# Performance work log

Hardware: AMD Instinct MI355X
Metric: run time of the kernel (lower is better)

## Reference

```python
import jax, jax.numpy as jnp
import numpy as np

N0 = 100000; E0 = 1600000; N1 = 100000; E1 = 1600000; G = 512
F0 = 93; F1 = 43
BN_EPS = 1e-5


def setup_inputs() -> dict:
    key = jax.random.key(0)
    ks = jax.random.split(key, 20)
    p = lambda i, shape: jax.random.normal(ks[i], shape, jnp.float32) * 0.02
    return {
        "x_0": jax.random.normal(ks[0], (N0, F0), jnp.float32),
        "x_1": jax.random.normal(ks[1], (N1, F1), jnp.float32),
        "edge_index_0": jax.random.randint(ks[2], (2, E0), 0, N0, jnp.int32),
        "edge_index_1": jax.random.randint(ks[3], (2, E1), 0, N1, jnp.int32),
        "batch_0": jnp.sort(jax.random.randint(ks[4], (N0,), 0, G, jnp.int32)),
        "batch_1": jnp.sort(jax.random.randint(ks[5], (N1,), 0, G, jnp.int32)),
        "w_c1": p(6, (F0, F0)), "b_c1": jnp.zeros((F0,), jnp.float32),
        "w_c2": p(7, (F0, F0 * 10)), "b_c2": jnp.zeros((F0 * 10,), jnp.float32),
        "w_c3": p(8, (F1, F1)), "b_c3": jnp.zeros((F1,), jnp.float32),
        "w_c4": p(9, (F1, F1 * 10)), "b_c4": jnp.zeros((F1 * 10,), jnp.float32),
        "g0_w1": p(10, (F0 * 10 * 2, 1024)), "g0_b1": jnp.zeros((1024,), jnp.float32),
        "g0_w2": p(11, (1024, 512)), "g0_b2": jnp.zeros((512,), jnp.float32),
        "g0_bn_g": jnp.ones((512,), jnp.float32), "g0_bn_b": jnp.zeros((512,), jnp.float32),
        "g1_w1": p(12, (F1 * 10 * 2, 1024)), "g1_b1": jnp.zeros((1024,), jnp.float32),
        "g1_w2": p(13, (1024, 512)), "g1_b2": jnp.zeros((512,), jnp.float32),
        "g1_bn_g": jnp.ones((512,), jnp.float32), "g1_bn_b": jnp.zeros((512,), jnp.float32),
        "f0_w1": p(14, (512, 256)), "f0_b1": jnp.zeros((256,), jnp.float32),
        "f0_w2": p(15, (256, 2)), "f0_b2": jnp.zeros((2,), jnp.float32),
        "f1_w1": p(16, (512, 256)), "f1_b1": jnp.zeros((256,), jnp.float32),
        "f1_w2": p(17, (256, 2)), "f1_b2": jnp.zeros((2,), jnp.float32),
    }


def gin_conv(x, edge_index, W, b):
    # GINConv(eps=0): nn(x + sum_{j->i} x_j); messages from src=edge_index[0] to dst=edge_index[1]
    agg = jax.ops.segment_sum(x[edge_index[0]], edge_index[1], num_segments=x.shape[0])
    return (x + agg) @ W + b


def pool_mean_max(x, batch):
    cnt = jax.ops.segment_sum(jnp.ones((x.shape[0], 1), x.dtype), batch, num_segments=G)
    mean = jax.ops.segment_sum(x, batch, num_segments=G) / jnp.maximum(cnt, 1.0)
    mx = jax.ops.segment_max(x, batch, num_segments=G)
    mx = jnp.where(cnt > 0, mx, 0.0)
    return jnp.concatenate([mean, mx], axis=1)


def batchnorm(x, g, b):
    m = x.mean(axis=0)
    v = x.var(axis=0)
    return g * (x - m) / jnp.sqrt(v + BN_EPS) + b


def branch(x, ei, batch, w_a, b_a, w_b, b_b, w1, b1, w2, b2, bn_g, bn_b):
    h = jax.nn.relu(gin_conv(x, ei, w_a, b_a))
    h = jax.nn.relu(gin_conv(h, ei, w_b, b_b))
    h = pool_mean_max(h, batch)              # [G, 2*10*F] ; PairNorm(mode='None') is identity
    h = jax.nn.relu(h @ w1 + b1)             # dropout: eval mode (identity)
    h = h @ w2 + b2
    return batchnorm(h, bn_g, bn_b)          # [G, 512]


def reference(x_0, x_1, edge_index_0, edge_index_1, batch_0, batch_1,
              w_c1, b_c1, w_c2, b_c2, w_c3, b_c3, w_c4, b_c4,
              g0_w1, g0_b1, g0_w2, g0_b2, g0_bn_g, g0_bn_b,
              g1_w1, g1_b1, g1_w2, g1_b2, g1_bn_g, g1_bn_b,
              f0_w1, f0_b1, f0_w2, f0_b2, f1_w1, f1_b1, f1_w2, f1_b2):
    x_g_0 = branch(x_0, edge_index_0, batch_0, w_c1, b_c1, w_c2, b_c2,
                   g0_w1, g0_b1, g0_w2, g0_b2, g0_bn_g, g0_bn_b)
    z = jax.nn.relu(x_g_0 @ f0_w1 + f0_b1) @ f0_w2 + f0_b2
    x_g_1 = branch(x_1, edge_index_1, batch_1, w_c3, b_c3, w_c4, b_c4,
                   g1_w1, g1_b1, g1_w2, g1_b2, g1_bn_g, g1_bn_b)
    z1 = jax.nn.relu(x_g_1 @ f1_w1 + f1_b1) @ f1_w2 + f1_b2
    return (z, x_g_0, x_g_1, z1)
```

## Files before the change

### kernel.cpp

```cpp
#include <hip/hip_runtime.h>
#include <hip/hip_bf16.h>

#define N0 100000
#define E0C 1600000
#define N1 100000
#define E1C 1600000
#define GCONST 512
#define F0C 93
#define F1C 43
#define OC0 (F0C * 10)
#define OC1 (F1C * 10)
#define BN_EPS 1e-5f
#define NBKT 391

typedef __attribute__((ext_vector_type(8))) short short8;
typedef __attribute__((ext_vector_type(4))) float floatx4;

static __device__ __forceinline__ unsigned short f2bf(float f) {
    unsigned u = __float_as_uint(f);
    unsigned r = (u + 0x7FFF + ((u >> 16) & 1)) >> 16;
    return (unsigned short)r;
}
static __device__ __forceinline__ float bf2f(unsigned short u) {
    return __uint_as_float(((unsigned)u) << 16);
}
static __device__ __forceinline__ void split_bf(float v, unsigned short& h, unsigned short& l) {
    h = f2bf(v);
    l = f2bf(v - bf2f(h));
}

__global__ __launch_bounds__(256) void bucket_count2_kernel(const int* __restrict__ ei0,
                                                            const int* __restrict__ ei1,
                                                            int E, int* __restrict__ btot2) {
    const int* ei = blockIdx.y ? ei1 : ei0;
    int* btot = btot2 + blockIdx.y * 512;
    __shared__ int h[NBKT];
    int t = threadIdx.x;
    for (int i = t; i < NBKT; i += 256) h[i] = 0;
    __syncthreads();
    int base = blockIdx.x * 2048;
#pragma unroll
    for (int i = 0; i < 8; ++i) {
        int e = base + i * 256 + t;
        if (e < E) atomicAdd(&h[ei[E + e] >> 8], 1);
    }
    __syncthreads();
    for (int i = t; i < NBKT; i += 256) {
        int c = h[i];
        if (c) atomicAdd(&btot[i], c);
    }
}

__global__ __launch_bounds__(512) void bucket_scan2_kernel(const int* __restrict__ btot2,
                                                           int* __restrict__ bbase2,
                                                           int* __restrict__ bcur2) {
    const int* btot = btot2 + blockIdx.x * 512;
    int* bbase = bbase2 + blockIdx.x * 512;
    int* bcur  = bcur2 + blockIdx.x * 512;
    __shared__ int sh[512];
    int t = threadIdx.x;
    int v = (t < NBKT) ? btot[t] : 0;
    sh[t] = v;
    __syncthreads();
    for (int o = 1; o < 512; o <<= 1) {
        int add = (t >= o) ? sh[t - o] : 0;
        __syncthreads();
        sh[t] += add;
        __syncthreads();
    }
    if (t < NBKT) {
        int ex = sh[t] - v;
        bbase[t] = ex;
        bcur[t] = ex;
    }
    if (t == NBKT) bbase[t] = sh[NBKT - 1];
}

__global__ __launch_bounds__(256) void edge_bucket2_kernel(const int* __restrict__ ei0,
                                                           const int* __restrict__ ei1,
                                                           int E, int* __restrict__ bcur2,
                                                           int2* __restrict__ st0,
                                                           int2* __restrict__ st1) {
    const int* ei = blockIdx.y ? ei1 : ei0;
    int* bcur = bcur2 + blockIdx.y * 512;
    int2* staging = blockIdx.y ? st1 : st0;
    __shared__ int hist[NBKT];
    __shared__ int gbase[NBKT];
    int t = threadIdx.x;
    for (int i = t; i < NBKT; i += 256) hist[i] = 0;
    __syncthreads();
    int base = blockIdx.x * 2048;
    int srcv[8], dstv[8];
#pragma unroll
    for (int i = 0; i < 8; ++i) {
        int e = base + i * 256 + t;
        if (e < E) { srcv[i] = ei[e]; dstv[i] = ei[E + e]; }
        else dstv[i] = -1;
    }
#pragma unroll
    for (int i = 0; i < 8; ++i)
        if (dstv[i] >= 0) atomicAdd(&hist[dstv[i] >> 8], 1);
    __syncthreads();
    for (int i = t; i < NBKT; i += 256) {
        int c = hist[i];
        gbase[i] = c ? atomicAdd(&bcur[i], c) : 0;
        hist[i] = 0;
    }
    __syncthreads();
#pragma unroll
    for (int i = 0; i < 8; ++i) {
        if (dstv[i] >= 0) {
            int b = dstv[i] >> 8;
            int lofs = atomicAdd(&hist[b], 1);
            staging[gbase[b] + lofs] = make_int2(srcv[i], dstv[i]);
        }
    }
}

static __device__ __forceinline__ void csr_build_dev(int b, const int2* __restrict__ staging,
                                                     const int* __restrict__ bbase, int N,
                                                     int* __restrict__ rowptr,
                                                     int* __restrict__ col) {
    __shared__ int h[256];
    __shared__ int sc[256];
    int t = threadIdx.x;
    int s = bbase[b], e = bbase[b + 1];
    h[t] = 0;
    __syncthreads();
    for (int i = s + t; i < e; i += 256)
        atomicAdd(&h[staging[i].y & 255], 1);
    __syncthreads();
    int v = h[t];
    sc[t] = v;
    __syncthreads();
    for (int o = 1; o < 256; o <<= 1) {
        int add = (t >= o) ? sc[t - o] : 0;
        __syncthreads();
        sc[t] += add;
        __syncthreads();
    }
    int ex = s + (sc[t] - v);
    int node = (b << 8) + t;
    if (node <= N) rowptr[node] = ex;
    __syncthreads();
    sc[t] = ex;
    __syncthreads();
    for (int i = s + t; i < e; i += 256) {
        int2 ed = staging[i];
        int pos = atomicAdd(&sc[ed.y & 255], 1);
        col[pos] = ed.x;
    }
}

__global__ __launch_bounds__(256) void misc_kernel(const int* __restrict__ bat0,
                                                   const int* __restrict__ bat1,
                                                   int* __restrict__ st0,
                                                   int* __restrict__ st1,
                                                   const float* __restrict__ Wc1,
                                                   const float* __restrict__ Wc2,
                                                   const float* __restrict__ Wc3,
                                                   const float* __restrict__ Wc4,
                                                   unsigned short* __restrict__ Ta0,
                                                   unsigned short* __restrict__ Tb0,
                                                   unsigned short* __restrict__ Ta1,
                                                   unsigned short* __restrict__ Tb1,
                                                   int* __restrict__ btot2,
                                                   unsigned short* __restrict__ p0h,
                                                   unsigned short* __restrict__ p0l,
                                                   unsigned short* __restrict__ p1h,
                                                   unsigned short* __restrict__ p1l) {
    int bid = blockIdx.x;
    int t = threadIdx.x;
    if (bid < 6) {
        int branch = bid / 3;
        const int* batch = branch ? bat1 : bat0;
        int* starts = branch ? st1 : st0;
        int g = (bid % 3) * 256 + t;
        if (g > GCONST) return;
        if (g == GCONST) { starts[GCONST] = N0; return; }
        int lo = 0, hi = N0;
        while (lo < hi) {
            int mid = (lo + hi) >> 1;
            if (batch[mid] < g) lo = mid + 1; else hi = mid;
        }
        starts[g] = lo;
    } else if (bid < 2054) {
        int idx = bid - 6;
        int cfg = idx >> 9;
        int c = (idx & 511) * 2 + (t >> 7);
        int k = t & 127;
        const float* W; unsigned short* T; int OCr, Fr, KP, RB;
        switch (cfg) {
            case 0:  W = Wc1; T = Ta0; OCr = 93;  Fr = 93; KP = 96; RB = 96;   break;
            case 1:  W = Wc2; T = Tb0; OCr = 930; Fr = 93; KP = 96; RB = 1024; break;
            case 2:  W = Wc3; T = Ta1; OCr = 43;  Fr = 43; KP = 64; RB = 48;   break;
            default: W = Wc4; T = Tb1; OCr = 430; Fr = 43; KP = 64; RB = 512;  break;
        }
        if (c >= RB || k >= KP) return;
        unsigned short v = 0;
        if (c < OCr && k < Fr) v = f2bf(W[(size_t)k * OCr + c]);
        T[(size_t)c * KP + k] = v;
    } else if (bid < 2058) {
        int i = (bid - 2054) * 256 + t;
        if (i < 1024) btot2[i] = 0;
    } else if (bid < 2178) {
        int i = (bid - 2058) * 256 + t;
        if (i >= GCONST * 60) return;
        int g = i / 60, c = 1860 + (i - g * 60);
        p0h[(size_t)g * 1920 + c] = 0;
        p0l[(size_t)g * 1920 + c] = 0;
    } else {
        int i = (bid - 2178) * 256 + t;
        if (i >= GCONST * 36) return;
        int g = i / 36, c = 860 + (i - g * 36);
        p1h[(size_t)g * 896 + c] = 0;
        p1l[(size_t)g * 896 + c] = 0;
    }
}

static __device__ __forceinline__ void wsplit_dev(int k0, int c0,
                                                  const float* __restrict__ W,
                                                  unsigned short* __restrict__ Th,
                                                  unsigned short* __restrict__ Tl,
                                                  int K, int N, int KP) {
    __shared__ float tile[32][33];
    int tx = threadIdx.x & 31, ty = threadIdx.x >> 5;
    for (int r = ty; r < 32; r += 8) {
        int k = k0 + r;
        tile[r][tx] = (k < K) ? W[(size_t)k * N + c0 + tx] : 0.f;
    }
    __syncthreads();
    for (int r = ty; r < 32; r += 8) {
        int c = c0 + r;
        float v = tile[tx][r];
        unsigned short h, l;
        split_bf(v, h, l);
        Th[(size_t)c * KP + k0 + tx] = h;
        Tl[(size_t)c * KP + k0 + tx] = l;
    }
}


template<int KP, int CH, int GR>
static __device__ __forceinline__ void gather_dev(int nb, unsigned short* __restrict__ t,
                                                  const unsigned short* __restrict__ x,
                                                  const int* __restrict__ rowptr,
                                                  const int* __restrict__ col, int N) {
    int wave = threadIdx.x >> 6, lane = threadIdx.x & 63;
    int node = nb * 4 + wave;
    if (node >= N) return;
    int g = lane / CH;
    int c = lane - g * CH;
    bool act = (g < GR);
    int s = rowptr[node], e = rowptr[node + 1];
    float acc[8] = {0.f, 0.f, 0.f, 0.f, 0.f, 0.f, 0.f, 0.f};
    int j = act ? (s - 1 + g) : e;
    int src0 = node;
    if (j >= s && j < e) src0 = col[j];
    while (j < e) {
        int jb = j + GR;
        int jc = jb + GR;
        int srcb = (jb < e) ? col[jb] : 0;
        int srcc = (jc < e) ? col[jc] : 0;
        short8 v0 = *(const short8*)(x + (size_t)src0 * KP + c * 8);
#pragma unroll
        for (int i = 0; i < 8; ++i) acc[i] += bf2f((unsigned short)v0[i]);
        if (jb < e) {
            short8 v1 = *(const short8*)(x + (size_t)srcb * KP + c * 8);
#pragma unroll
            for (int i = 0; i < 8; ++i) acc[i] += bf2f((unsigned short)v1[i]);
        }
        j = jc; src0 = srcc;
    }
    if (GR == 8) {
#pragma unroll
        for (int i = 0; i < 8; ++i) {
            float v = acc[i];
            v += __shfl_xor(v, 8);
            v += __shfl_xor(v, 16);
            v += __shfl_xor(v, 32);
            acc[i] = v;
        }
    } else {
#pragma unroll
        for (int i = 0; i < 8; ++i) {
            float v = acc[i];
            float v1 = __shfl(v, lane + CH);
            float v2 = __shfl(v, lane + 2 * CH);
            float v3 = __shfl(v, lane + 3 * CH);
            float v4 = __shfl(v, lane + 4 * CH);
            acc[i] = v + v1 + v2 + v3 + v4;
        }
    }
    if (lane < CH) {
        short8 o;
#pragma unroll
        for (int i = 0; i < 8; ++i) o[i] = (short)f2bf(acc[i]);
        *(short8*)(t + (size_t)node * KP + lane * 8) = o;
    }
}

template<int KP, int KS, int NT>
static __device__ __forceinline__ void conv1_dev(int nb, const unsigned short* __restrict__ t,
                                                 const unsigned short* __restrict__ Wt,
                                                 const float* __restrict__ bias,
                                                 unsigned short* __restrict__ y,
                                                 int NC, int N) {
    int wave = threadIdx.x >> 6, lane = threadIdx.x & 63;
    int quad = lane >> 4, l15 = lane & 15;
    int r0 = (nb * 4 + wave) * 16;
    const short8 z8 = {0, 0, 0, 0, 0, 0, 0, 0};
    short8 a[KS];
    int arow = r0 + l15;
#pragma unroll
    for (int ks = 0; ks < KS; ++ks)
        a[ks] = (arow < N) ? *(const short8*)(t + (size_t)arow * KP + ks * 32 + quad * 8) : z8;
#pragma unroll
    for (int nt = 0; nt < NT; ++nt) {
        int colb = nt * 16 + l15;
        floatx4 c = {0.f, 0.f, 0.f, 0.f};
#pragma unroll
        for (int ks = 0; ks < KS; ++ks) {
            short8 b = *(const short8*)(Wt + (size_t)colb * KP + ks * 32 + quad * 8);
            c = __builtin_amdgcn_mfma_f32_16x16x32_bf16(a[ks], b, c, 0, 0, 0);
// ... 131 lines not shown
    int col0 = c0 + l15, col1 = c0 + 16 + l15;
    float bc0 = bias[col0], bc1 = bias[col1];
#pragma unroll
    for (int r = 0; r < 4; ++r) {
        int row = r0 + quad * 4 + r;
        float v0 = acc0[r] + bc0;
        float v1 = acc1[r] + bc1;
        if (MODE != 1) { v0 = fmaxf(v0, 0.f); v1 = fmaxf(v1, 0.f); }
        if (MODE == 0) {
            unsigned short h, l;
            split_bf(v0, h, l);
            Ch[(size_t)row * Ncols + col0] = h; Cl[(size_t)row * Ncols + col0] = l;
            split_bf(v1, h, l);
            Ch[(size_t)row * Ncols + col1] = h; Cl[(size_t)row * Ncols + col1] = l;
        } else {
            Cf[(size_t)row * Ncols + col0] = v0;
            Cf[(size_t)row * Ncols + col1] = v1;
        }
    }
}

static __device__ __forceinline__ void bn_dev(int c, const float* __restrict__ p,
                                              const float* __restrict__ gamma,
                                              const float* __restrict__ beta,
                                              float* __restrict__ outp,
                                              unsigned short* __restrict__ oh,
                                              unsigned short* __restrict__ ol) {
    __shared__ float ls[256], ls2[256];
    int t = threadIdx.x;
    float v0 = p[(size_t)t * 512 + c];
    float v1 = p[(size_t)(t + 256) * 512 + c];
    ls[t] = v0 + v1;
    ls2[t] = v0 * v0 + v1 * v1;
    __syncthreads();
    for (int st = 128; st > 0; st >>= 1) {
        if (t < st) { ls[t] += ls[t + st]; ls2[t] += ls2[t + st]; }
        __syncthreads();
    }
    if (t == 0) {
        float m = ls[0] / 512.f;
        float var = ls2[0] / 512.f - m * m;
        ls[0] = m;
        ls2[0] = 1.f / sqrtf(var + BN_EPS);
    }
    __syncthreads();
    float m = ls[0], iv = ls2[0];
    float g = gamma[c], b = beta[c];
    float w0 = g * (v0 - m) * iv + b;
    float w1 = g * (v1 - m) * iv + b;
    outp[(size_t)t * 512 + c] = w0;
    outp[(size_t)(t + 256) * 512 + c] = w1;
    unsigned short h, l;
    split_bf(w0, h, l);
    oh[(size_t)t * 512 + c] = h; ol[(size_t)t * 512 + c] = l;
    split_bf(w1, h, l);
    oh[(size_t)(t + 256) * 512 + c] = h; ol[(size_t)(t + 256) * 512 + c] = l;
}

static __device__ __forceinline__ void head2_dev(int nb, const float* __restrict__ h,
                                                 const float* __restrict__ w2,
                                                 const float* __restrict__ b2,
                                                 float* __restrict__ z, int M) {
    int wave = threadIdx.x >> 6, lane = threadIdx.x & 63;
    int row = nb * 4 + wave;
    if (row >= M) return;
    float4 hv = *(const float4*)(h + (size_t)row * 256 + lane * 4);
    const float* wp = w2 + lane * 8;
    float s0 = hv.x * wp[0] + hv.y * wp[2] + hv.z * wp[4] + hv.w * wp[6];
    float s1 = hv.x * wp[1] + hv.y * wp[3] + hv.z * wp[5] + hv.w * wp[7];
#pragma unroll
    for (int offd = 32; offd >= 1; offd >>= 1) {
        s0 += __shfl_down(s0, offd);
        s1 += __shfl_down(s1, offd);
    }
    if (lane == 0) {
        z[(size_t)row * 2 + 0] = s0 + b2[0];
        z[(size_t)row * 2 + 1] = s1 + b2[1];
    }
}


__global__ __launch_bounds__(256) void f0_kernel(const int2* __restrict__ st0,
                                                 const int2* __restrict__ st1,
                                                 const int* __restrict__ bbase2,
                                                 int* __restrict__ rp0, int* __restrict__ rp1,
                                                 int* __restrict__ c0, int* __restrict__ c1,
                                                 unsigned short* __restrict__ xb0,
                                                 const float* __restrict__ x0,
                                                 unsigned short* __restrict__ xb1,
                                                 const float* __restrict__ x1) {
    int bid = blockIdx.x;
    if (bid < 2 * NBKT) {
        int branch = bid >= NBKT;
        csr_build_dev(branch ? bid - NBKT : bid,
                      branch ? st1 : st0, bbase2 + branch * 512, N0,
                      branch ? rp1 : rp0, branch ? c1 : c0);
    } else if (bid < 2 * NBKT + 50000) {
        int b = bid - 2 * NBKT;
        int node = b * 2 + (threadIdx.x >> 7);
        int f = threadIdx.x & 127;
        if (node < N0 && f < 96)
            xb0[(size_t)node * 96 + f] = (f < 93) ? f2bf(x0[(size_t)node * 93 + f]) : (unsigned short)0;
    } else {
        int b = bid - 2 * NBKT - 50000;
        int node = b * 4 + (threadIdx.x >> 6);
        int f = threadIdx.x & 63;
        if (node < N1)
            xb1[(size_t)node * 64 + f] = (f < 43) ? f2bf(x1[(size_t)node * 43 + f]) : (unsigned short)0;
    }
}

__global__ __launch_bounds__(256) void f1_kernel(unsigned short* __restrict__ tb,
                                                 const unsigned short* __restrict__ xb0,
                                                 const int* __restrict__ rowptr0,
                                                 const int* __restrict__ col0,
                                                 const float* g0_w1, const float* g0_w2,
                                                 const float* f0_w1,
                                                 const float* g1_w1, const float* g1_w2,
                                                 const float* f1_w1,
                                                 unsigned short* bt1h0, unsigned short* bt1l0,
                                                 unsigned short* bt2h0, unsigned short* bt2l0,
                                                 unsigned short* bt3h0, unsigned short* bt3l0,
                                                 unsigned short* bt1h1, unsigned short* bt1l1,
                                                 unsigned short* bt2h1, unsigned short* bt2l1,
                                                 unsigned short* bt3h1, unsigned short* bt3l1) {
    int bid = blockIdx.x;
    if (bid < 25000) {
        gather_dev<96, 12, 5>(bid, tb, xb0, rowptr0, col0, N0);
        return;
    }
    int w = bid - 25000;
    if (w < 1920)      wsplit_dev((w % 60) * 32, (w / 60) * 32, g0_w1, bt1h0, bt1l0, 1860, 1024, 1920);
    else if (w < 2432) { w -= 1920; wsplit_dev((w % 32) * 32, (w / 32) * 32, g0_w2, bt2h0, bt2l0, 1024, 512, 1024); }
    else if (w < 2560) { w -= 2432; wsplit_dev((w % 16) * 32, (w / 16) * 32, f0_w1, bt3h0, bt3l0, 512, 256, 512); }
    else if (w < 3456) { w -= 2560; wsplit_dev((w % 28) * 32, (w / 28) * 32, g1_w1, bt1h1, bt1l1, 860, 1024, 896); }
    else if (w < 3968) { w -= 3456; wsplit_dev((w % 32) * 32, (w / 32) * 32, g1_w2, bt2h1, bt2l1, 1024, 512, 1024); }
    else               { w -= 3968; wsplit_dev((w % 16) * 32, (w / 16) * 32, f1_w1, bt3h1, bt3l1, 512, 256, 512); }
}

__global__ __launch_bounds__(256) void f2_kernel(unsigned short* __restrict__ t1,
                                                 const unsigned short* __restrict__ xb1,
                                                 const int* __restrict__ rowptr1,
                                                 const int* __restrict__ col1,
                                                 const unsigned short* __restrict__ tb,
                                                 const unsigned short* __restrict__ wt_a0,
                                                 const float* __restrict__ b_c1,
                                                 unsigned short* __restrict__ yb) {
    int bid = blockIdx.x;
    if (bid < 25000)
        gather_dev<64, 8, 8>(bid, t1, xb1, rowptr1, col1, N1);
    else
        conv1_dev<96, 3, 6>(bid - 25000, tb, wt_a0, b_c1, yb, 93, N0);
}

__global__ __launch_bounds__(256) void f3_kernel(unsigned short* __restrict__ tb,
                                                 const unsigned short* __restrict__ yb,
                                                 const int* __restrict__ rowptr0,
                                                 const int* __restrict__ col0,
                                                 const unsigned short* __restrict__ t1,
                                                 const unsigned short* __restrict__ wt_a1,
                                                 const float* __restrict__ b_c3,
                                                 unsigned short* __restrict__ y1) {
    int bid = blockIdx.x;
    if (bid < 25000)
        gather_dev<96, 12, 5>(bid, tb, yb, rowptr0, col0, N0);
    else
        conv1_dev<64, 2, 3>(bid - 25000, t1, wt_a1, b_c3, y1, 43, N1);
}

__global__ __launch_bounds__(256) void f4_kernel(unsigned short* __restrict__ t1,
                                                 const unsigned short* __restrict__ y1,
                                                 const int* __restrict__ rowptr1,
                                                 const int* __restrict__ col1,
                                                 const unsigned short* __restrict__ tb,
                                                 const unsigned short* __restrict__ wt_b0,
                                                 const float* __restrict__ b_c2,
                                                 const int* __restrict__ starts0,
                                                 unsigned short* __restrict__ p0h,
                                                 unsigned short* __restrict__ p0l) {
    int bid = blockIdx.x;
    if (bid < 25000)
        gather_dev<64, 8, 8>(bid, t1, y1, rowptr1, col1, N1);
    else {
        int b = bid - 25000;
        conv2_pool_dev<96, 3>(b & 3, b >> 2, tb, wt_b0, b_c2, starts0, p0h, p0l, OC0, 1920);
    }
}

__global__ __launch_bounds__(256) void f5_kernel(const unsigned short* __restrict__ t1,
                                                 const unsigned short* __restrict__ wt_b1,
                                                 const float* __restrict__ b_c4,
                                                 const int* __restrict__ starts1,
                                                 unsigned short* __restrict__ p1h,
                                                 unsigned short* __restrict__ p1l,
                                                 const unsigned short* __restrict__ p0h,
                                                 const unsigned short* __restrict__ p0l,
                                                 const unsigned short* __restrict__ bt1h0,
                                                 const unsigned short* __restrict__ bt1l0,
                                                 const float* __restrict__ g0_b1,
                                                 unsigned short* __restrict__ m1h0,
                                                 unsigned short* __restrict__ m1l0) {
    int bid = blockIdx.x;
    if (bid < 1024)
        conv2_pool_dev<64, 2>(bid & 1, bid >> 1, t1, wt_b1, b_c4, starts1, p1h, p1l, OC1, 896);
    else {
        int b = bid - 1024;
        gemm3x_dev<0>(b & 15, b >> 4, 16, p0h, p0l, bt1h0, bt1l0, g0_b1,
                      nullptr, m1h0, m1l0, 1920);
    }
}

__global__ __launch_bounds__(256) void f6_kernel(const unsigned short* __restrict__ p1h,
                                                 const unsigned short* __restrict__ p1l,
                                                 const unsigned short* __restrict__ bt1h1,
                                                 const unsigned short* __restrict__ bt1l1,
                                                 const float* __restrict__ g1_b1,
                                                 unsigned short* __restrict__ m1h1,
                                                 unsigned short* __restrict__ m1l1,
                                                 const unsigned short* __restrict__ m1h0,
                                                 const unsigned short* __restrict__ m1l0,
                                                 const unsigned short* __restrict__ bt2h0,
                                                 const unsigned short* __restrict__ bt2l0,
                                                 const float* __restrict__ g0_b2,
                                                 float* __restrict__ pbn0) {
    int bid = blockIdx.x;
    if (bid < 256)
        gemm3x_dev<0>(bid & 15, bid >> 4, 16, p1h, p1l, bt1h1, bt1l1, g1_b1,
                      nullptr, m1h1, m1l1, 896);
    else {
        int b = bid - 256;
        gemm3x_dev<1>(b & 7, b >> 3, 8, m1h0, m1l0, bt2h0, bt2l0, g0_b2,
                      pbn0, nullptr, nullptr, 1024);
    }
}

__global__ __launch_bounds__(256) void f7_kernel(const unsigned short* __restrict__ m1h1,
                                                 const unsigned short* __restrict__ m1l1,
                                                 const unsigned short* __restrict__ bt2h1,
                                                 const unsigned short* __restrict__ bt2l1,
                                                 const float* __restrict__ g1_b2,
                                                 float* __restrict__ pbn1,
                                                 const float* __restrict__ pbn0,
                                                 const float* __restrict__ g0_bn_g,
                                                 const float* __restrict__ g0_bn_b,
                                                 float* __restrict__ out_xg0,
                                                 unsigned short* __restrict__ xgh0,
                                                 unsigned short* __restrict__ xgl0) {
    int bid = blockIdx.x;
    if (bid < 128)
        gemm3x_dev<1>(bid & 7, bid >> 3, 8, m1h1, m1l1, bt2h1, bt2l1, g1_b2,
                      pbn1, nullptr, nullptr, 1024);
    else
        bn_dev(bid - 128, pbn0, g0_bn_g, g0_bn_b, out_xg0, xgh0, xgl0);
}

__global__ __launch_bounds__(256) void f8_kernel(const float* __restrict__ pbn1,
                                                 const float* __restrict__ g1_bn_g,
                                                 const float* __restrict__ g1_bn_b,
                                                 float* __restrict__ out_xg1,
                                                 unsigned short* __restrict__ xgh1,
                                                 unsigned short* __restrict__ xgl1,
                                                 const unsigned short* __restrict__ xgh0,
                                                 const unsigned short* __restrict__ xgl0,
                                                 const unsigned short* __restrict__ bt3h0,
                                                 const unsigned short* __restrict__ bt3l0,
                                                 const float* __restrict__ f0_b1,
                                                 float* __restrict__ hbuf0) {
    int bid = blockIdx.x;
    if (bid < 512)
        bn_dev(bid, pbn1, g1_bn_g, g1_bn_b, out_xg1, xgh1, xgl1);
    else {
        int b = bid - 512;
        gemm3x_dev<2>(b & 3, b >> 2, 4, xgh0, xgl0, bt3h0, bt3l0, f0_b1,
                      hbuf0, nullptr, nullptr, 512);
    }
}

__global__ __launch_bounds__(256) void f9_kernel(const unsigned short* __restrict__ xgh1,
                                                 const unsigned short* __restrict__ xgl1,
                                                 const unsigned short* __restrict__ bt3h1,
                                                 const unsigned short* __restrict__ bt3l1,
                                                 const float* __restrict__ f1_b1,
                                                 float* __restrict__ hbuf1,
                                                 const float* __restrict__ hbuf0,
                                                 const float* __restrict__ f0_w2,
                                                 const float* __restrict__ f0_b2,
                                                 float* __restrict__ out_z) {
    int bid = blockIdx.x;
    if (bid < 64)
        gemm3x_dev<2>(bid & 3, bid >> 2, 4, xgh1, xgl1, bt3h1, bt3l1, f1_b1,
                      hbuf1, nullptr, nullptr, 512);
    else
        head2_dev(bid - 64, hbuf0, f0_w2, f0_b2, out_z, GCONST);
}

__global__ __launch_bounds__(256) void head2_kernel(const float* __restrict__ h,
                                                    const float* __restrict__ w2,
                                                    const float* __restrict__ b2,
                                                    float* __restrict__ z, int M) {
    head2_dev(blockIdx.x, h, w2, b2, z, M);
}

static inline int ceildiv(int a, int b) { return (a + b - 1) / b; }

extern "C" void kernel_launch(void* const* d_in, const int* in_sizes, int n_in,
                              void* d_out, int out_size, void* d_ws, size_t ws_size,
                              hipStream_t stream) {
    const float* x0   = (const float*)d_in[0];
    const float* x1   = (const float*)d_in[1];
    const int*   ei0  = (const int*)d_in[2];
    const int*   ei1  = (const int*)d_in[3];
    const int*   bat0 = (const int*)d_in[4];
    const int*   bat1 = (const int*)d_in[5];
    const float* w_c1 = (const float*)d_in[6];
    const float* b_c1 = (const float*)d_in[7];
    const float* w_c2 = (const float*)d_in[8];
    const float* b_c2 = (const float*)d_in[9];
    const float* w_c3 = (const float*)d_in[10];
    const float* b_c3 = (const float*)d_in[11];
    const float* w_c4 = (const float*)d_in[12];
    const float* b_c4 = (const float*)d_in[13];
    const float* g0_w1 = (const float*)d_in[14];
    const float* g0_b1 = (const float*)d_in[15];
    const float* g0_w2 = (const float*)d_in[16];
    const float* g0_b2 = (const float*)d_in[17];
    const float* g0_bn_g = (const float*)d_in[18];
    const float* g0_bn_b = (const float*)d_in[19];
    const float* g1_w1 = (const float*)d_in[20];
    const float* g1_b1 = (const float*)d_in[21];
    const float* g1_w2 = (const float*)d_in[22];
    const float* g1_b2 = (const float*)d_in[23];
    const float* g1_bn_g = (const float*)d_in[24];
    const float* g1_bn_b = (const float*)d_in[25];
    const float* f0_w1 = (const float*)d_in[26];
    const float* f0_b1 = (const float*)d_in[27];
    const float* f0_w2 = (const float*)d_in[28];
    const float* f0_b2 = (const float*)d_in[29];
    const float* f1_w1 = (const float*)d_in[30];
    const float* f1_b1 = (const float*)d_in[31];
    const float* f1_w2 = (const float*)d_in[32];
    const float* f1_b2 = (const float*)d_in[33];

    float* out = (float*)d_out;
    float* out_z   = out;
    float* out_xg0 = out + 1024;
    float* out_xg1 = out + 1024 + 262144;
    float* out_z1  = out + 1024 + 262144 + 262144;

    float* ws = (float*)d_ws;
    size_t off = 0;
    auto alloc = [&](size_t n) { float* p = ws + off; off += n; return p; };
    unsigned short* xb0 = (unsigned short*)alloc((size_t)N0 * 96 / 2);
    unsigned short* xb1 = (unsigned short*)alloc((size_t)N1 * 64 / 2);
    unsigned short* tb  = (unsigned short*)alloc((size_t)N0 * 96 / 2);
    unsigned short* yb  = (unsigned short*)alloc((size_t)N0 * 96 / 2);
    unsigned short* wt_a0 = (unsigned short*)alloc(96 * 96 / 2);
    unsigned short* wt_b0 = (unsigned short*)alloc(1024 * 96 / 2);
    unsigned short* wt_a1 = (unsigned short*)alloc(48 * 64 / 2);
    unsigned short* wt_b1 = (unsigned short*)alloc(512 * 64 / 2);
    unsigned short* bt1h0 = (unsigned short*)alloc((size_t)1024 * 1920 / 2);
    unsigned short* bt1l0 = (unsigned short*)alloc((size_t)1024 * 1920 / 2);
    unsigned short* bt2h0 = (unsigned short*)alloc((size_t)512 * 1024 / 2);
    unsigned short* bt2l0 = (unsigned short*)alloc((size_t)512 * 1024 / 2);
    unsigned short* bt3h0 = (unsigned short*)alloc((size_t)256 * 512 / 2);
    unsigned short* bt3l0 = (unsigned short*)alloc((size_t)256 * 512 / 2);
    unsigned short* bt1h1 = (unsigned short*)alloc((size_t)1024 * 896 / 2);
    unsigned short* bt1l1 = (unsigned short*)alloc((size_t)1024 * 896 / 2);
    unsigned short* bt2h1 = (unsigned short*)alloc((size_t)512 * 1024 / 2);
    unsigned short* bt2l1 = (unsigned short*)alloc((size_t)512 * 1024 / 2);
    unsigned short* bt3h1 = (unsigned short*)alloc((size_t)256 * 512 / 2);
    unsigned short* bt3l1 = (unsigned short*)alloc((size_t)256 * 512 / 2);
    unsigned short* m1h0 = (unsigned short*)alloc((size_t)512 * 1024 / 2);
    unsigned short* m1l0 = (unsigned short*)alloc((size_t)512 * 1024 / 2);
    unsigned short* m1h1 = (unsigned short*)alloc((size_t)512 * 1024 / 2);
    unsigned short* m1l1 = (unsigned short*)alloc((size_t)512 * 1024 / 2);
    unsigned short* xgh0 = (unsigned short*)alloc((size_t)512 * 512 / 2);
    unsigned short* xgl0 = (unsigned short*)alloc((size_t)512 * 512 / 2);
    unsigned short* xgh1 = (unsigned short*)alloc((size_t)512 * 512 / 2);
    unsigned short* xgl1 = (unsigned short*)alloc((size_t)512 * 512 / 2);
    unsigned short* p0h = (unsigned short*)alloc((size_t)512 * 1920 / 2);
    unsigned short* p0l = (unsigned short*)alloc((size_t)512 * 1920 / 2);
    unsigned short* p1h = (unsigned short*)alloc((size_t)512 * 896 / 2);
    unsigned short* p1l = (unsigned short*)alloc((size_t)512 * 896 / 2);
    float* pbn0  = alloc((size_t)512 * 512);
    float* pbn1  = alloc((size_t)512 * 512);
    float* hbuf0 = alloc((size_t)512 * 256);
    float* hbuf1 = alloc((size_t)512 * 256);
    int* btot2  = (int*)alloc(1024);
    int* bbase2 = (int*)alloc(1024);
    int* bcur2  = (int*)alloc(1024);
    int* rowptr0 = (int*)alloc(100016);
    int* col0    = (int*)alloc(E0C);
    int* rowptr1 = (int*)alloc(100016);
    int* col1    = (int*)alloc(E1C);
    int* starts0 = (int*)alloc(520);
    int* starts1 = (int*)alloc(520);
    int2* staging0 = (int2*)tb;
    int2* staging1 = (int2*)yb;
    unsigned short* t1 = xb0;
    unsigned short* y1 = xb1;

    const int EB = ceildiv(E0C, 2048);

    misc_kernel<<<2250, 256, 0, stream>>>(bat0, bat1, starts0, starts1,
                                          w_c1, w_c2, w_c3, w_c4,
                                          wt_a0, wt_b0, wt_a1, wt_b1,
                                          btot2, p0h, p0l, p1h, p1l);
    bucket_count2_kernel<<<dim3(EB, 2), 256, 0, stream>>>(ei0, ei1, E0C, btot2);
    bucket_scan2_kernel<<<2, 512, 0, stream>>>(btot2, bbase2, bcur2);
    edge_bucket2_kernel<<<dim3(EB, 2), 256, 0, stream>>>(ei0, ei1, E0C, bcur2, staging0, staging1);
    f0_kernel<<<2 * NBKT + 50000 + 25000, 256, 0, stream>>>(
        staging0, staging1, bbase2, rowptr0, rowptr1, col0, col1,
        xb0, x0, xb1, x1);

    f1_kernel<<<25000 + 4096, 256, 0, stream>>>(
        tb, xb0, rowptr0, col0,
        g0_w1, g0_w2, f0_w1, g1_w1, g1_w2, f1_w1,
        bt1h0, bt1l0, bt2h0, bt2l0, bt3h0, bt3l0,
        bt1h1, bt1l1, bt2h1, bt2l1, bt3h1, bt3l1);
    f2_kernel<<<25000 + 1563, 256, 0, stream>>>(t1, xb1, rowptr1, col1,
                                                tb, wt_a0, b_c1, yb);
    f3_kernel<<<25000 + 1563, 256, 0, stream>>>(tb, yb, rowptr0, col0,
                                                t1, wt_a1, b_c3, y1);
    f4_kernel<<<25000 + 2048, 256, 0, stream>>>(t1, y1, rowptr1, col1,
                                                tb, wt_b0, b_c2, starts0, p0h, p0l);
    f5_kernel<<<1024 + 256, 256, 0, stream>>>(t1, wt_b1, b_c4, starts1, p1h, p1l,
                                              p0h, p0l, bt1h0, bt1l0, g0_b1, m1h0, m1l0);
    f6_kernel<<<256 + 128, 256, 0, stream>>>(p1h, p1l, bt1h1, bt1l1, g1_b1, m1h1, m1l1,
                                             m1h0, m1l0, bt2h0, bt2l0, g0_b2, pbn0);
    f7_kernel<<<128 + 512, 256, 0, stream>>>(m1h1, m1l1, bt2h1, bt2l1, g1_b2, pbn1,
                                             pbn0, g0_bn_g, g0_bn_b, out_xg0, xgh0, xgl0);
    f8_kernel<<<512 + 64, 256, 0, stream>>>(pbn1, g1_bn_g, g1_bn_b, out_xg1, xgh1, xgl1,
                                            xgh0, xgl0, bt3h0, bt3l0, f0_b1, hbuf0);
    f9_kernel<<<64 + 128, 256, 0, stream>>>(xgh1, xgl1, bt3h1, bt3l1, f1_b1, hbuf1,
                                            hbuf0, f0_w2, f0_b2, out_z);
    head2_kernel<<<GCONST / 4, 256, 0, stream>>>(hbuf1, f1_w2, f1_b2, out_z1, GCONST);
}
```

Baseline: 730.7 us.

## Drop bucket-count pass via fixed-slab staging and regroup tail kernels by branch

```diff
diff --git a/kernel.cpp b/kernel.cpp
--- a/kernel.cpp
+++ b/kernel.cpp
@@ -12,6 +12,7 @@
 #define OC1 (F1C * 10)
 #define BN_EPS 1e-5f
 #define NBKT 391
+#define SLAB 6016
 
 typedef __attribute__((ext_vector_type(8))) short short8;
 typedef __attribute__((ext_vector_type(4))) float floatx4;
@@ -29,146 +30,11 @@
     l = f2bf(v - bf2f(h));
 }
 
-__global__ __launch_bounds__(256) void bucket_count2_kernel(const int* __restrict__ ei0,
-                                                            const int* __restrict__ ei1,
-                                                            int E, int* __restrict__ btot2) {
-    const int* ei = blockIdx.y ? ei1 : ei0;
-    int* btot = btot2 + blockIdx.y * 512;
-    __shared__ int h[NBKT];
-    int t = threadIdx.x;
-    for (int i = t; i < NBKT; i += 256) h[i] = 0;
-    __syncthreads();
-    int base = blockIdx.x * 2048;
-#pragma unroll
-    for (int i = 0; i < 8; ++i) {
-        int e = base + i * 256 + t;
-        if (e < E) atomicAdd(&h[ei[E + e] >> 8], 1);
-    }
-    __syncthreads();
-    for (int i = t; i < NBKT; i += 256) {
-        int c = h[i];
-        if (c) atomicAdd(&btot[i], c);
-    }
-}
-
-__global__ __launch_bounds__(512) void bucket_scan2_kernel(const int* __restrict__ btot2,
-                                                           int* __restrict__ bbase2,
-                                                           int* __restrict__ bcur2) {
-    const int* btot = btot2 + blockIdx.x * 512;
-    int* bbase = bbase2 + blockIdx.x * 512;
-    int* bcur  = bcur2 + blockIdx.x * 512;
-    __shared__ int sh[512];
-    int t = threadIdx.x;
-    int v = (t < NBKT) ? btot[t] : 0;
-    sh[t] = v;
-    __syncthreads();
-    for (int o = 1; o < 512; o <<= 1) {
-        int add = (t >= o) ? sh[t - o] : 0;
-        __syncthreads();
-        sh[t] += add;
-        __syncthreads();
-    }
-    if (t < NBKT) {
-        int ex = sh[t] - v;
-        bbase[t] = ex;
-        bcur[t] = ex;
-    }
-    if (t == NBKT) bbase[t] = sh[NBKT - 1];
-}
-
-__global__ __launch_bounds__(256) void edge_bucket2_kernel(const int* __restrict__ ei0,
-                                                           const int* __restrict__ ei1,
-                                                           int E, int* __restrict__ bcur2,
-                                                           int2* __restrict__ st0,
-                                                           int2* __restrict__ st1) {
-    const int* ei = blockIdx.y ? ei1 : ei0;
-    int* bcur = bcur2 + blockIdx.y * 512;
-    int2* staging = blockIdx.y ? st1 : st0;
-    __shared__ int hist[NBKT];
-    __shared__ int gbase[NBKT];
-    int t = threadIdx.x;
-    for (int i = t; i < NBKT; i += 256) hist[i] = 0;
-    __syncthreads();
-    int base = blockIdx.x * 2048;
-    int srcv[8], dstv[8];
-#pragma unroll
-    for (int i = 0; i < 8; ++i) {
-        int e = base + i * 256 + t;
-        if (e < E) { srcv[i] = ei[e]; dstv[i] = ei[E + e]; }
-        else dstv[i] = -1;
-    }
-#pragma unroll
-    for (int i = 0; i < 8; ++i)
-        if (dstv[i] >= 0) atomicAdd(&hist[dstv[i] >> 8], 1);
-    __syncthreads();
-    for (int i = t; i < NBKT; i += 256) {
-        int c = hist[i];
-        gbase[i] = c ? atomicAdd(&bcur[i], c) : 0;
-        hist[i] = 0;
-    }
-    __syncthreads();
-#pragma unroll
-    for (int i = 0; i < 8; ++i) {
-        if (dstv[i] >= 0) {
-            int b = dstv[i] >> 8;
-            int lofs = atomicAdd(&hist[b], 1);
-            staging[gbase[b] + lofs] = make_int2(srcv[i], dstv[i]);
-        }
-    }
-}
-
-static __device__ __forceinline__ void csr_build_dev(int b, const int2* __restrict__ staging,
-                                                     const int* __restrict__ bbase, int N,
-                                                     int* __restrict__ rowptr,
-                                                     int* __restrict__ col) {
-    __shared__ int h[256];
-    __shared__ int sc[256];
-    int t = threadIdx.x;
-    int s = bbase[b], e = bbase[b + 1];
-    h[t] = 0;
-    __syncthreads();
-    for (int i = s + t; i < e; i += 256)
-        atomicAdd(&h[staging[i].y & 255], 1);
-    __syncthreads();
-    int v = h[t];
-    sc[t] = v;
-    __syncthreads();
-    for (int o = 1; o < 256; o <<= 1) {
-        int add = (t >= o) ? sc[t - o] : 0;
-        __syncthreads();
-        sc[t] += add;
-        __syncthreads();
-    }
-    int ex = s + (sc[t] - v);
-    int node = (b << 8) + t;
-    if (node <= N) rowptr[node] = ex;
-    __syncthreads();
-    sc[t] = ex;
-    __syncthreads();
-    for (int i = s + t; i < e; i += 256) {
-        int2 ed = staging[i];
-        int pos = atomicAdd(&sc[ed.y & 255], 1);
-        col[pos] = ed.x;
-    }
-}
-
 __global__ __launch_bounds__(256) void misc_kernel(const int* __restrict__ bat0,
                                                    const int* __restrict__ bat1,
                                                    int* __restrict__ st0,
                                                    int* __restrict__ st1,
-                                                   const float* __restrict__ Wc1,
-                                                   const float* __restrict__ Wc2,
-                                                   const float* __restrict__ Wc3,
-                                                   const float* __restrict__ Wc4,
-                                                   unsigned short* __restrict__ Ta0,
-                                                   unsigned short* __restrict__ Tb0,
-                                                   unsigned short* __restrict__ Ta1,
-                                                   unsigned short* __restrict__ Tb1,
-                                                   int* __restrict__ btot2,
-                                                   unsigned short* __restrict__ p0h,
-                                                   unsigned short* __restrict__ p0l,
-                                                   unsigned short* __restrict__ p1h,
-                                                   unsigned short* __restrict__ p1l) {
+                                                   int* __restrict__ bcur2) {
     int bid = blockIdx.x;
     int t = threadIdx.x;
     if (bid < 6) {
@@ -184,8 +50,71 @@
             if (batch[mid] < g) lo = mid + 1; else hi = mid;
         }
         starts[g] = lo;
-    } else if (bid < 2054) {
-        int idx = bid - 6;
+    } else {
+        for (int i = t; i < 1024; i += 256) {
+            if (i < NBKT) bcur2[i] = i * SLAB;
+            else if (i >= 512 && i < 512 + NBKT) bcur2[i] = (i - 512) * SLAB;
+        }
+    }
+}
+
+__global__ __launch_bounds__(256) void edge_bucket2_kernel(const int* __restrict__ ei0,
+                                                           const int* __restrict__ ei1,
+                                                           int E, int* __restrict__ bcur2,
+                                                           int2* __restrict__ st0,
+                                                           int2* __restrict__ st1,
+                                                           const float* __restrict__ Wc1,
+                                                           const float* __restrict__ Wc2,
+                                                           const float* __restrict__ Wc3,
+                                                           const float* __restrict__ Wc4,
+                                                           unsigned short* __restrict__ Ta0,
+                                                           unsigned short* __restrict__ Tb0,
+                                                           unsigned short* __restrict__ Ta1,
+                                                           unsigned short* __restrict__ Tb1,
+                                                           unsigned short* __restrict__ p0h,
+                                                           unsigned short* __restrict__ p0l,
+                                                           unsigned short* __restrict__ p1h,
+                                                           unsigned short* __restrict__ p1l) {
+    int bid = blockIdx.x;
+    int t = threadIdx.x;
+    if (bid < 1564) {
+        int branch = bid >= 782;
+        int blk = branch ? bid - 782 : bid;
+        const int* ei = branch ? ei1 : ei0;
+        int* bcur = bcur2 + branch * 512;
+        int2* staging = branch ? st1 : st0;
+        __shared__ int hist[NBKT];
+        __shared__ int gbase[NBKT];
+        for (int i = t; i < NBKT; i += 256) hist[i] = 0;
+        __syncthreads();
+        int base = blk * 2048;
+        int srcv[8], dstv[8];
+#pragma unroll
+        for (int i = 0; i < 8; ++i) {
+            int e = base + i * 256 + t;
+            if (e < E) { srcv[i] = ei[e]; dstv[i] = ei[E + e]; }
+            else dstv[i] = -1;
+        }
+#pragma unroll
+        for (int i = 0; i < 8; ++i)
+            if (dstv[i] >= 0) atomicAdd(&hist[dstv[i] >> 8], 1);
+        __syncthreads();
+        for (int i = t; i < NBKT; i += 256) {
+            int c = hist[i];
+            gbase[i] = c ? atomicAdd(&bcur[i], c) : 0;
+            hist[i] = 0;
+        }
+        __syncthreads();
+#pragma unroll
+        for (int i = 0; i < 8; ++i) {
+            if (dstv[i] >= 0) {
+                int b = dstv[i] >> 8;
+                int lofs = atomicAdd(&hist[b], 1);
+                staging[gbase[b] + lofs] = make_int2(srcv[i], dstv[i]);
+            }
+        }
+    } else if (bid < 3612) {
+        int idx = bid - 1564;
         int cfg = idx >> 9;
         int c = (idx & 511) * 2 + (t >> 7);
         int k = t & 127;
@@ -200,21 +129,74 @@
         unsigned short v = 0;
         if (c < OCr && k < Fr) v = f2bf(W[(size_t)k * OCr + c]);
         T[(size_t)c * KP + k] = v;
-    } else if (bid < 2058) {
-        int i = (bid - 2054) * 256 + t;
-        if (i < 1024) btot2[i] = 0;
-    } else if (bid < 2178) {
-        int i = (bid - 2058) * 256 + t;
+    } else if (bid < 3732) {
+        int i = (bid - 3612) * 256 + t;
         if (i >= GCONST * 60) return;
         int g = i / 60, c = 1860 + (i - g * 60);
         p0h[(size_t)g * 1920 + c] = 0;
         p0l[(size_t)g * 1920 + c] = 0;
     } else {
-        int i = (bid - 2178) * 256 + t;
+        int i = (bid - 3732) * 256 + t;
         if (i >= GCONST * 36) return;
         int g = i / 36, c = 860 + (i - g * 36);
         p1h[(size_t)g * 896 + c] = 0;
         p1l[(size_t)g * 896 + c] = 0;
+    }
+}
+
+__global__ __launch_bounds__(512) void bucket_scan2_kernel(const int* __restrict__ bcur2,
+                                                           int* __restrict__ bbase2) {
+    const int* bcur = bcur2 + blockIdx.x * 512;
+    int* bbase = bbase2 + blockIdx.x * 512;
+    __shared__ int sh[512];
+    int t = threadIdx.x;
+    int cnt = (t < NBKT) ? bcur[t] - t * SLAB : 0;
+    sh[t] = cnt;
+    __syncthreads();
+    for (int o = 1; o < 512; o <<= 1) {
+        int add = (t >= o) ? sh[t - o] : 0;
+        __syncthreads();
+        sh[t] += add;
+        __syncthreads();
+    }
+    if (t <= NBKT) bbase[t] = sh[t] - cnt;
+}
+
+static __device__ __forceinline__ void csr_build_dev(int b, const int2* __restrict__ staging,
+                                                     const int* __restrict__ bcur,
+                                                     const int* __restrict__ bbase, int N,
+                                                     int* __restrict__ rowptr,
+                                                     int* __restrict__ col) {
+    __shared__ int h[256];
+    __shared__ int sc[256];
+    int t = threadIdx.x;
+    int sl = b * SLAB;
+    int se = bcur[b];
+    int go = bbase[b];
+    h[t] = 0;
+    __syncthreads();
+    for (int i = sl + t; i < se; i += 256)
+        atomicAdd(&h[staging[i].y & 255], 1);
+    __syncthreads();
+    int v = h[t];
+    sc[t] = v;
+    __syncthreads();
+    for (int o = 1; o < 256; o <<= 1) {
+        int add = (t >= o) ? sc[t - o] : 0;
+        __syncthreads();
+        sc[t] += add;
+        __syncthreads();
+    }
+    int ex = go + (sc[t] - v);
+    int node = (b << 8) + t;
+    if (node <= N) rowptr[node] = ex;
+    __syncthreads();
+    sc[t] = ex;
+    __syncthreads();
+    for (int i = sl + t; i < se; i += 256) {
+        int2 ed = staging[i];
+        int pos = atomicAdd(&sc[ed.y & 255], 1);
+        col[pos] = ed.x;
     }
 }
 
@@ -239,7 +221,6 @@
         Tl[(size_t)c * KP + k0 + tx] = l;
     }
 }
-
 
 template<int KP, int CH, int GR>
 static __device__ __forceinline__ void gather_dev(int nb, unsigned short* __restrict__ t,
@@ -537,6 +518,7 @@
 
 __global__ __launch_bounds__(256) void f0_kernel(const int2* __restrict__ st0,
                                                  const int2* __restrict__ st1,
+                                                 const int* __restrict__ bcur2,
                                                  const int* __restrict__ bbase2,
                                                  int* __restrict__ rp0, int* __restrict__ rp1,
                                                  int* __restrict__ c0, int* __restrict__ c1,
@@ -548,7 +530,8 @@
     if (bid < 2 * NBKT) {
         int branch = bid >= NBKT;
         csr_build_dev(branch ? bid - NBKT : bid,
-                      branch ? st1 : st0, bbase2 + branch * 512, N0,
+                      branch ? st1 : st0,
+                      bcur2 + branch * 512, bbase2 + branch * 512, N0,
                       branch ? rp1 : rp0, branch ? c1 : c0);
     } else if (bid < 2 * NBKT + 50000) {
         int b = bid - 2 * NBKT;
@@ -626,134 +609,139 @@
 __global__ __launch_bounds__(256) void f4_kernel(unsigned short* __restrict__ t1,
                                                  const unsigned short* __restrict__ y1,
                                                  const int* __restrict__ rowptr1,
-                                                 const int* __restrict__ col1,
-                                                 const unsigned short* __restrict__ tb,
+                                                 const int* __restrict__ col1) {
+    gather_dev<64, 8, 8>(blockIdx.x, t1, y1, rowptr1, col1, N1);
+}
+
+__global__ __launch_bounds__(256) void f5_kernel(const unsigned short* __restrict__ tb,
                                                  const unsigned short* __restrict__ wt_b0,
                                                  const float* __restrict__ b_c2,
                                                  const int* __restrict__ starts0,
                                                  unsigned short* __restrict__ p0h,
-                                                 unsigned short* __restrict__ p0l) {
-    int bid = blockIdx.x;
-    if (bid < 25000)
-        gather_dev<64, 8, 8>(bid, t1, y1, rowptr1, col1, N1);
-    else {
-        int b = bid - 25000;
-        conv2_pool_dev<96, 3>(b & 3, b >> 2, tb, wt_b0, b_c2, starts0, p0h, p0l, OC0, 1920);
-    }
-}
-
-__global__ __launch_bounds__(256) void f5_kernel(const unsigned short* __restrict__ t1,
+                                                 unsigned short* __restrict__ p0l,
+                                                 const unsigned short* __restrict__ t1,
                                                  const unsigned short* __restrict__ wt_b1,
                                                  const float* __restrict__ b_c4,
                                                  const int* __restrict__ starts1,
                                                  unsigned short* __restrict__ p1h,
-                                                 unsigned short* __restrict__ p1l,
-                                                 const unsigned short* __restrict__ p0h,
+                                                 unsigned short* __restrict__ p1l) {
+    int bid = blockIdx.x;
+    if (bid < 2048) {
+        int b = bid;
+        int g = (b & 7) | ((b >> 5) << 3);
+        int cb = (b >> 3) & 3;
+        conv2_pool_dev<96, 3>(cb, g, tb, wt_b0, b_c2, starts0, p0h, p0l, OC0, 1920);
+    } else {
+        int b = bid - 2048;
+        int g = (b & 7) | ((b >> 4) << 3);
+        int cb = (b >> 3) & 1;
+        conv2_pool_dev<64, 2>(cb, g, t1, wt_b1, b_c4, starts1, p1h, p1l, OC1, 896);
+    }
+}
+
+__global__ __launch_bounds__(256) void f6_kernel(const unsigned short* __restrict__ p0h,
                                                  const unsigned short* __restrict__ p0l,
                                                  const unsigned short* __restrict__ bt1h0,
                                                  const unsigned short* __restrict__ bt1l0,
                                                  const float* __restrict__ g0_b1,
                                                  unsigned short* __restrict__ m1h0,
-                                                 unsigned short* __restrict__ m1l0) {
-    int bid = blockIdx.x;
-    if (bid < 1024)
-        conv2_pool_dev<64, 2>(bid & 1, bid >> 1, t1, wt_b1, b_c4, starts1, p1h, p1l, OC1, 896);
-    else {
-        int b = bid - 1024;
-        gemm3x_dev<0>(b & 15, b >> 4, 16, p0h, p0l, bt1h0, bt1l0, g0_b1,
-                      nullptr, m1h0, m1l0, 1920);
-    }
-}
-
-__global__ __launch_bounds__(256) void f6_kernel(const unsigned short* __restrict__ p1h,
+                                                 unsigned short* __restrict__ m1l0,
+                                                 const unsigned short* __restrict__ p1h,
                                                  const unsigned short* __restrict__ p1l,
                                                  const unsigned short* __restrict__ bt1h1,
                                                  const unsigned short* __restrict__ bt1l1,
                                                  const float* __restrict__ g1_b1,
                                                  unsigned short* __restrict__ m1h1,
-                                                 unsigned short* __restrict__ m1l1,
-                                                 const unsigned short* __restrict__ m1h0,
+                                                 unsigned short* __restrict__ m1l1) {
+    int bid = blockIdx.x;
+    if (bid < 256)
+        gemm3x_dev<0>(bid & 15, bid >> 4, 16, p0h, p0l, bt1h0, bt1l0, g0_b1,
+                      nullptr, m1h0, m1l0, 1920);
+    else {
+        int b = bid - 256;
+        gemm3x_dev<0>(b & 15, b >> 4, 16, p1h, p1l, bt1h1, bt1l1, g1_b1,
+                      nullptr, m1h1, m1l1, 896);
+    }
+}
+
+__global__ __launch_bounds__(256) void f7_kernel(const unsigned short* __restrict__ m1h0,
                                                  const unsigned short* __restrict__ m1l0,
                                                  const unsigned short* __restrict__ bt2h0,
                                                  const unsigned short* __restrict__ bt2l0,
                                                  const float* __restrict__ g0_b2,
-                                                 float* __restrict__ pbn0) {
-    int bid = blockIdx.x;
-    if (bid < 256)
-        gemm3x_dev<0>(bid & 15, bid >> 4, 16, p1h, p1l, bt1h1, bt1l1, g1_b1,
-                      nullptr, m1h1, m1l1, 896);
-    else {
-        int b = bid - 256;
-        gemm3x_dev<1>(b & 7, b >> 3, 8, m1h0, m1l0, bt2h0, bt2l0, g0_b2,
-                      pbn0, nullptr, nullptr, 1024);
-    }
-}
-
-__global__ __launch_bounds__(256) void f7_kernel(const unsigned short* __restrict__ m1h1,
+                                                 float* __restrict__ pbn0,
+                                                 const unsigned short* __restrict__ m1h1,
                                                  const unsigned short* __restrict__ m1l1,
                                                  const unsigned short* __restrict__ bt2h1,
                                                  const unsigned short* __restrict__ bt2l1,
                                                  const float* __restrict__ g1_b2,
-                                                 float* __restrict__ pbn1,
-                                                 const float* __restrict__ pbn0,
+                                                 float* __restrict__ pbn1) {
+    int bid = blockIdx.x;
+    if (bid < 128)
+        gemm3x_dev<1>(bid & 7, bid >> 3, 8, m1h0, m1l0, bt2h0, bt2l0, g0_b2,
+                      pbn0, nullptr, nullptr, 1024);
+    else {
+        int b = bid - 128;
+        gemm3x_dev<1>(b & 7, b >> 3, 8, m1h1, m1l1, bt2h1, bt2l1, g1_b2,
+                      pbn1, nullptr, nullptr, 1024);
+    }
+}
+
+__global__ __launch_bounds__(256) void f8_kernel(const float* __restrict__ pbn0,
                                                  const float* __restrict__ g0_bn_g,
                                                  const float* __restrict__ g0_bn_b,
                                                  float* __restrict__ out_xg0,
                                                  unsigned short* __restrict__ xgh0,
-                                                 unsigned short* __restrict__ xgl0) {
-    int bid = blockIdx.x;
-    if (bid < 128)
-        gemm3x_dev<1>(bid & 7, bid >> 3, 8, m1h1, m1l1, bt2h1, bt2l1, g1_b2,
-                      pbn1, nullptr, nullptr, 1024);
-    else
-        bn_dev(bid - 128, pbn0, g0_bn_g, g0_bn_b, out_xg0, xgh0, xgl0);
-}
-
-__global__ __launch_bounds__(256) void f8_kernel(const float* __restrict__ pbn1,
+                                                 unsigned short* __restrict__ xgl0,
+                                                 const float* __restrict__ pbn1,
                                                  const float* __restrict__ g1_bn_g,
                                                  const float* __restrict__ g1_bn_b,
                                                  float* __restrict__ out_xg1,
                                                  unsigned short* __restrict__ xgh1,
-                                                 unsigned short* __restrict__ xgl1,
-                                                 const unsigned short* __restrict__ xgh0,
+                                                 unsigned short* __restrict__ xgl1) {
+    int bid = blockIdx.x;
+    if (bid < 512)
+        bn_dev(bid, pbn0, g0_bn_g, g0_bn_b, out_xg0, xgh0, xgl0);
+    else
+        bn_dev(bid - 512, pbn1, g1_bn_g, g1_bn_b, out_xg1, xgh1, xgl1);
+}
+
+__global__ __launch_bounds__(256) void f9_kernel(const unsigned short* __restrict__ xgh0,
                                                  const unsigned short* __restrict__ xgl0,
                                                  const unsigned short* __restrict__ bt3h0,
                                                  const unsigned short* __restrict__ bt3l0,
                                                  const float* __restrict__ f0_b1,
-                                                 float* __restrict__ hbuf0) {
-    int bid = blockIdx.x;
-    if (bid < 512)
-        bn_dev(bid, pbn1, g1_bn_g, g1_bn_b, out_xg1, xgh1, xgl1);
-    else {
-        int b = bid - 512;
-        gemm3x_dev<2>(b & 3, b >> 2, 4, xgh0, xgl0, bt3h0, bt3l0, f0_b1,
-                      hbuf0, nullptr, nullptr, 512);
-    }
-}
-
-__global__ __launch_bounds__(256) void f9_kernel(const unsigned short* __restrict__ xgh1,
+                                                 float* __restrict__ hbuf0,
+                                                 const unsigned short* __restrict__ xgh1,
                                                  const unsigned short* __restrict__ xgl1,
                                                  const unsigned short* __restrict__ bt3h1,
                                                  const unsigned short* __restrict__ bt3l1,
                                                  const float* __restrict__ f1_b1,
-                                                 float* __restrict__ hbuf1,
-                                                 const float* __restrict__ hbuf0,
-                                                 const float* __restrict__ f0_w2,
-                                                 const float* __restrict__ f0_b2,
-                                                 float* __restrict__ out_z) {
+                                                 float* __restrict__ hbuf1) {
     int bid = blockIdx.x;
     if (bid < 64)
-        gemm3x_dev<2>(bid & 3, bid >> 2, 4, xgh1, xgl1, bt3h1, bt3l1, f1_b1,
+        gemm3x_dev<2>(bid & 3, bid >> 2, 4, xgh0, xgl0, bt3h0, bt3l0, f0_b1,
+                      hbuf0, nullptr, nullptr, 512);
+    else {
+        int b = bid - 64;
+        gemm3x_dev<2>(b & 3, b >> 2, 4, xgh1, xgl1, bt3h1, bt3l1, f1_b1,
                       hbuf1, nullptr, nullptr, 512);
+    }
+}
+
+__global__ __launch_bounds__(256) void f10_kernel(const float* __restrict__ hbuf0,
+                                                  const float* __restrict__ f0_w2,
+                                                  const float* __restrict__ f0_b2,
+                                                  float* __restrict__ out_z,
+                                                  const float* __restrict__ hbuf1,
+                                                  const float* __restrict__ f1_w2,
+                                                  const float* __restrict__ f1_b2,
+                                                  float* __restrict__ out_z1) {
+    int bid = blockIdx.x;
+    if (bid < 128)
+        head2_dev(bid, hbuf0, f0_w2, f0_b2, out_z, GCONST);
     else
-        head2_dev(bid - 64, hbuf0, f0_w2, f0_b2, out_z, GCONST);
-}
-
-__global__ __launch_bounds__(256) void head2_kernel(const float* __restrict__ h,
-                                                    const float* __restrict__ w2,
-                                                    const float* __restrict__ b2,
-                                                    float* __restrict__ z, int M) {
-    head2_dev(blockIdx.x, h, w2, b2, z, M);
+        head2_dev(bid - 128, hbuf1, f1_w2, f1_b2, out_z1, GCONST);
 }
 
 static inline int ceildiv(int a, int b) { return (a + b - 1) / b; }
@@ -841,7 +829,6 @@
     float* pbn1  = alloc((size_t)512 * 512);
     float* hbuf0 = alloc((size_t)512 * 256);
     float* hbuf1 = alloc((size_t)512 * 256);
-    int* btot2  = (int*)alloc(1024);
     int* bbase2 = (int*)alloc(1024);
     int* bcur2  = (int*)alloc(1024);
     int* rowptr0 = (int*)alloc(100016);
@@ -855,17 +842,15 @@
     unsigned short* t1 = xb0;
     unsigned short* y1 = xb1;
 
-    const int EB = ceildiv(E0C, 2048);
-
-    misc_kernel<<<2250, 256, 0, stream>>>(bat0, bat1, starts0, starts1,
-                                          w_c1, w_c2, w_c3, w_c4,
-                                          wt_a0, wt_b0, wt_a1, wt_b1,
-                                          btot2, p0h, p0l, p1h, p1l);
-    bucket_count2_kernel<<<dim3(EB, 2), 256, 0, stream>>>(ei0, ei1, E0C, btot2);
-    bucket_scan2_kernel<<<2, 512, 0, stream>>>(btot2, bbase2, bcur2);
-    edge_bucket2_kernel<<<dim3(EB, 2), 256, 0, stream>>>(ei0, ei1, E0C, bcur2, staging0, staging1);
+    misc_kernel<<<7, 256, 0, stream>>>(bat0, bat1, starts0, starts1, bcur2);
+    edge_bucket2_kernel<<<3804, 256, 0, stream>>>(ei0, ei1, E0C, bcur2,
+                                                  staging0, staging1,
+                                                  w_c1, w_c2, w_c3, w_c4,
+                                                  wt_a0, wt_b0, wt_a1, wt_b1,
+                                                  p0h, p0l, p1h, p1l);
+    bucket_scan2_kernel<<<2, 512, 0, stream>>>(bcur2, bbase2);
     f0_kernel<<<2 * NBKT + 50000 + 25000, 256, 0, stream>>>(
-        staging0, staging1, bbase2, rowptr0, rowptr1, col0, col1,
+        staging0, staging1, bcur2, bbase2, rowptr0, rowptr1, col0, col1,
         xb0, x0, xb1, x1);
 
     f1_kernel<<<25000 + 4096, 256, 0, stream>>>(
@@ -877,17 +862,17 @@
                                                 tb, wt_a0, b_c1, yb);
     f3_kernel<<<25000 + 1563, 256, 0, stream>>>(tb, yb, rowptr0, col0,
                                                 t1, wt_a1, b_c3, y1);
-    f4_kernel<<<25000 + 2048, 256, 0, stream>>>(t1, y1, rowptr1, col1,
-                                                tb, wt_b0, b_c2, starts0, p0h, p0l);
-    f5_kernel<<<1024 + 256, 256, 0, stream>>>(t1, wt_b1, b_c4, starts1, p1h, p1l,
-                                              p0h, p0l, bt1h0, bt1l0, g0_b1, m1h0, m1l0);
-    f6_kernel<<<256 + 128, 256, 0, stream>>>(p1h, p1l, bt1h1, bt1l1, g1_b1, m1h1, m1l1,
-                                             m1h0, m1l0, bt2h0, bt2l0, g0_b2, pbn0);
-    f7_kernel<<<128 + 512, 256, 0, stream>>>(m1h1, m1l1, bt2h1, bt2l1, g1_b2, pbn1,
-                                             pbn0, g0_bn_g, g0_bn_b, out_xg0, xgh0, xgl0);
-    f8_kernel<<<512 + 64, 256, 0, stream>>>(pbn1, g1_bn_g, g1_bn_b, out_xg1, xgh1, xgl1,
-                                            xgh0, xgl0, bt3h0, bt3l0, f0_b1, hbuf0);
-    f9_kernel<<<64 + 128, 256, 0, stream>>>(xgh1, xgl1, bt3h1, bt3l1, f1_b1, hbuf1,
-                                            hbuf0, f0_w2, f0_b2, out_z);
-    head2_kernel<<<GCONST / 4, 256, 0, stream>>>(hbuf1, f1_w2, f1_b2, out_z1, GCONST);
-}
+    f4_kernel<<<25000, 256, 0, stream>>>(t1, y1, rowptr1, col1);
+    f5_kernel<<<2048 + 1024, 256, 0, stream>>>(tb, wt_b0, b_c2, starts0, p0h, p0l,
+                                               t1, wt_b1, b_c4, starts1, p1h, p1l);
+    f6_kernel<<<256 + 256, 256, 0, stream>>>(p0h, p0l, bt1h0, bt1l0, g0_b1, m1h0, m1l0,
+                                             p1h, p1l, bt1h1, bt1l1, g1_b1, m1h1, m1l1);
+    f7_kernel<<<128 + 128, 256, 0, stream>>>(m1h0, m1l0, bt2h0, bt2l0, g0_b2, pbn0,
+                                             m1h1, m1l1, bt2h1, bt2l1, g1_b2, pbn1);
+    f8_kernel<<<512 + 512, 256, 0, stream>>>(pbn0, g0_bn_g, g0_bn_b, out_xg0, xgh0, xgl0,
+                                             pbn1, g1_bn_g, g1_bn_b, out_xg1, xgh1, xgl1);
+    f9_kernel<<<64 + 64, 256, 0, stream>>>(xgh0, xgl0, bt3h0, bt3l0, f0_b1, hbuf0,
+                                           xgh1, xgl1, bt3h1, bt3l1, f1_b1, hbuf1);
+    f10_kernel<<<128 + 128, 256, 0, stream>>>(hbuf0, f0_w2, f0_b2, out_z,
+                                              hbuf1, f1_w2, f1_b2, out_z1);
+}
```

After: 665.8 us. 1.1x faster.
